# Performance work log

Hardware: AMD Instinct MI355X
Metric: run time of the kernel (lower is better)

The kernel has to match this reference:

```python
import math
import jax, jax.numpy as jnp
import numpy as np


def kaiser_sinc_filter1d(cutoff, half_width, kernel_size):
    even = kernel_size % 2 == 0
    half_size = kernel_size // 2
    delta_f = 4 * half_width
    A = 2.285 * (half_size - 1) * math.pi * delta_f + 7.95
    if A > 50.0:
        beta = 0.1102 * (A - 8.7)
    elif A >= 21.0:
        beta = 0.5842 * (A - 21) ** 0.4 + 0.07886 * (A - 21.0)
    else:
        beta = 0.0
    window = np.kaiser(kernel_size, beta)  # == torch.kaiser_window(periodic=False)
    if even:
        time = np.arange(-half_size, half_size) + 0.5
    else:
        time = np.arange(kernel_size) - half_size
    if cutoff == 0:
        filt = np.zeros_like(time)
    else:
        filt = 2 * cutoff * window * np.sinc(2 * cutoff * time)
        filt = filt / filt.sum()
    return jnp.asarray(filt, dtype=jnp.float32)  # [K]


def _depthwise_conv1d(x, filt, stride, lhs_dilation, padding):
    # x: [B, C, T]; filt: [K] shared across channels (groups=C depthwise)
    C = x.shape[1]
    K = filt.shape[0]
    w = jnp.broadcast_to(filt.reshape(1, 1, K), (C, 1, K))
    return jax.lax.conv_general_dilated(
        x, w,
        window_strides=(stride,),
        padding=[padding],
        lhs_dilation=(lhs_dilation,),
        dimension_numbers=("NCH", "OIH", "NCH"),
        feature_group_count=C,
    )


UP = 2
DOWN = 2
UP_K = 12
DOWN_K = 12


def setup_inputs() -> dict:
    key = jax.random.key(0)
    B, C, T = 16, 512, 4096
    x = jax.random.normal(key, (B, C, T), dtype=jnp.float32)
    alpha = jnp.zeros((1, C, 1), dtype=jnp.float32)
    beta = jnp.zeros((1, C, 1), dtype=jnp.float32)
    up_filter = kaiser_sinc_filter1d(0.5 / UP, 0.6 / UP, UP_K)
    down_filter = kaiser_sinc_filter1d(0.5 / DOWN, 0.6 / DOWN, DOWN_K)
    return {"x": x, "alpha": alpha, "beta": beta,
            "up_filter": up_filter, "down_filter": down_filter}


def reference(x, alpha, beta, up_filter, down_filter):
    # ---- UpSample1d(ratio=UP, kernel_size=UP_K) ----
    pad = UP_K // UP - 1
    pad_left = pad * UP + (UP_K - UP) // 2
    pad_right = pad * UP + (UP_K - UP + 1) // 2
    xp = jnp.pad(x, ((0, 0), (0, 0), (pad, pad)), mode="edge")  # replicate pad
    # conv_transpose1d(stride=UP) == conv with lhs_dilation=UP, full padding, flipped kernel
    y = UP * _depthwise_conv1d(xp, up_filter[::-1], stride=1,
                               lhs_dilation=UP, padding=(UP_K - 1, UP_K - 1))
    y = y[..., pad_left:-pad_right]  # [B, C, UP*T]

    # ---- SnakeBeta ----
    y = y + 1.0 / (jnp.exp(beta) + 1e-9) * jnp.square(jnp.sin(y * jnp.exp(alpha)))

    # ---- DownSample1d(ratio=DOWN, kernel_size=DOWN_K) via LowPassFilter1d ----
    even = DOWN_K % 2 == 0
    dpl = DOWN_K // 2 - int(even)
    dpr = DOWN_K // 2
    yp = jnp.pad(y, ((0, 0), (0, 0), (dpl, dpr)), mode="edge")
    out = _depthwise_conv1d(yp, down_filter, stride=DOWN,
                            lhs_dilation=1, padding=(0, 0))  # [B, C, T]
    return out
```

## Files before the change

### kernel.cpp

```cpp
#include <hip/hip_runtime.h>
#include <math.h>


#define T_LEN 4096
#define TILE  1024
#define NT    256
#define BPR   (T_LEN / TILE)
#define XT4   260
#define NG    258
#define PL4   260

__global__ __launch_bounds__(NT) void aa_act_kernel(
    const float* __restrict__ x,
    const float* __restrict__ alpha,
    const float* __restrict__ beta,
    const float* __restrict__ upf,
    const float* __restrict__ downf,
    float* __restrict__ out,
    int C)
{
    __shared__ __align__(16) float sx[XT4 * 4];
    __shared__ __align__(16) float sE[PL4 * 4];
    __shared__ __align__(16) float sO[PL4 * 4];

    const int tid = threadIdx.x;
    const int blk = blockIdx.x;
    const int row = blk >> 2;
    const int o0  = (blk & (BPR - 1)) * TILE;
    const int c   = row % C;

    const float* __restrict__ xr = x + (size_t)row * T_LEN;
    float* __restrict__ outr = out + (size_t)row * T_LEN;

    float u[12], d[12];
#pragma unroll
    for (int i = 0; i < 12; ++i) { u[i] = upf[i]; d[i] = downf[i]; }

    const float ea = __expf(alpha[c]);
    const float rb = 1.0f / (__expf(beta[c]) + 1e-9f);

    const bool eblk = (o0 == 0) || (o0 + TILE == T_LEN);
    for (int i4 = tid; i4 < XT4; i4 += NT) {
        int gi = o0 - 8 + 4 * i4;
        float4 v;
        if (!eblk || (unsigned)gi <= (unsigned)(T_LEN - 4)) {
            v = *(const float4*)(xr + gi);
        } else {
            v.x = xr[min(max(gi + 0, 0), T_LEN - 1)];
            v.y = xr[min(max(gi + 1, 0), T_LEN - 1)];
            v.z = xr[min(max(gi + 2, 0), T_LEN - 1)];
            v.w = xr[min(max(gi + 3, 0), T_LEN - 1)];
        }
        ((float4*)sx)[i4] = v;
    }
    __syncthreads();

    const float4* sx4 = (const float4*)sx;
    for (int g = tid; g < NG; g += NT) {
        float4 A = sx4[g], Bv = sx4[g + 1], Cv = sx4[g + 2];
        float f[12] = { A.x, A.y, A.z, A.w, Bv.x, Bv.y, Bv.z, Bv.w,
                        Cv.x, Cv.y, Cv.z, Cv.w };
        float eo[4], oo[4];
#pragma unroll
        for (int r = 0; r < 4; ++r) {
            float yo = f[r + 3] * u[10];
            yo = fmaf(f[r + 4], u[8], yo);
            yo = fmaf(f[r + 5], u[6], yo);
            yo = fmaf(f[r + 6], u[4], yo);
            yo = fmaf(f[r + 7], u[2], yo);
            yo = fmaf(f[r + 8], u[0], yo);
            float ye = f[r + 3] * u[11];
            ye = fmaf(f[r + 4], u[9], ye);
            ye = fmaf(f[r + 5], u[7], ye);
            ye = fmaf(f[r + 6], u[5], ye);
            ye = fmaf(f[r + 7], u[3], ye);
            ye = fmaf(f[r + 8], u[1], ye);
            yo *= 2.0f; ye *= 2.0f;
            float so_ = __sinf(yo * ea);
            float se_ = __sinf(ye * ea);
            oo[r] = fmaf(rb * so_, so_, yo);
            eo[r] = fmaf(rb * se_, se_, ye);
        }
        float4 ev; ev.x = eo[0]; ev.y = eo[1]; ev.z = eo[2]; ev.w = eo[3];
        float4 ov; ov.x = oo[0]; ov.y = oo[1]; ov.z = oo[2]; ov.w = oo[3];
        ((float4*)sE)[g] = ev;
        ((float4*)sO)[g] = ov;
    }
    __syncthreads();

    if (o0 == 0) {
        float L = sE[2];
        if (tid < 2) sE[tid] = L;
        if (tid < 3) sO[tid] = L;
    }
    if (o0 + TILE == T_LEN) {
        float R = sO[TILE + 2];
        if (tid < 6) sE[TILE + 2 + tid] = R;
        if (tid < 5) sO[TILE + 3 + tid] = R;
    }
    __syncthreads();

    const float4* e4 = (const float4*)sE;
    const float4* q4 = (const float4*)sO;
    float4 E0 = e4[tid], E1 = e4[tid + 1], E2 = e4[tid + 2];
    float4 O0 = q4[tid], O1 = q4[tid + 1], O2 = q4[tid + 2];
    float e[12] = { E0.x, E0.y, E0.z, E0.w, E1.x, E1.y, E1.z, E1.w,
                    E2.x, E2.y, E2.z, E2.w };
    float o_[12] = { O0.x, O0.y, O0.z, O0.w, O1.x, O1.y, O1.z, O1.w,
                     O2.x, O2.y, O2.z, O2.w };
    float acc[4];
#pragma unroll
    for (int r = 0; r < 4; ++r) {
        float a = e[r] * d[1];
        a = fmaf(e[r + 1], d[3],  a);
        a = fmaf(e[r + 2], d[5],  a);
        a = fmaf(e[r + 3], d[7],  a);
        a = fmaf(e[r + 4], d[9],  a);
        a = fmaf(e[r + 5], d[11], a);
        a = fmaf(o_[r],     d[0],  a);
        a = fmaf(o_[r + 1], d[2],  a);
        a = fmaf(o_[r + 2], d[4],  a);
        a = fmaf(o_[r + 3], d[6],  a);
        a = fmaf(o_[r + 4], d[8],  a);
        a = fmaf(o_[r + 5], d[10], a);
        acc[r] = a;
    }
    float4 o4; o4.x = acc[0]; o4.y = acc[1]; o4.z = acc[2]; o4.w = acc[3];
    ((float4*)(outr + o0))[tid] = o4;
}

extern "C" void kernel_launch(void* const* d_in, const int* in_sizes, int n_in,
                              void* d_out, int out_size, void* d_ws, size_t ws_size,
                              hipStream_t stream) {
    const float* x     = (const float*)d_in[0];
    const float* alpha = (const float*)d_in[1];
    const float* beta  = (const float*)d_in[2];
    const float* upf   = (const float*)d_in[3];
    const float* downf = (const float*)d_in[4];
    float* out = (float*)d_out;

    const int C    = in_sizes[1];
    const int rows = in_sizes[0] / T_LEN;

    dim3 grid(rows * BPR), block(NT);
    hipLaunchKernelGGL(aa_act_kernel, grid, block, 0, stream,
                       x, alpha, beta, upf, downf, out, C);
}
```

Measured before the change: 243.6 us.

## Compute each 16-output window per thread in registers, dropping shared memory

Result: slower. 270.4 us (+11.0%).

```diff
diff --git a/kernel.cpp b/kernel.cpp
--- a/kernel.cpp
+++ b/kernel.cpp
@@ -3,12 +3,8 @@
 
 
 #define T_LEN 4096
-#define TILE  1024
 #define NT    256
-#define BPR   (T_LEN / TILE)
-#define XT4   260
-#define NG    258
-#define PL4   260
+#define W     16
 
 __global__ __launch_bounds__(NT) void aa_act_kernel(
     const float* __restrict__ x,
@@ -19,98 +15,72 @@
     float* __restrict__ out,
     int C)
 {
-    __shared__ __align__(16) float sx[XT4 * 4];
-    __shared__ __align__(16) float sE[PL4 * 4];
-    __shared__ __align__(16) float sO[PL4 * 4];
-
-    const int tid = threadIdx.x;
-    const int blk = blockIdx.x;
-    const int row = blk >> 2;
-    const int o0  = (blk & (BPR - 1)) * TILE;
+    const int t   = threadIdx.x;
+    const int row = blockIdx.x;
     const int c   = row % C;
+    const int o0  = t * W;
 
     const float* __restrict__ xr = x + (size_t)row * T_LEN;
-    float* __restrict__ outr = out + (size_t)row * T_LEN;
+    float* __restrict__ outr     = out + (size_t)row * T_LEN;
 
-    float u[12], d[12];
+    float ue[6], uo[6], d[12];
 #pragma unroll
-    for (int i = 0; i < 12; ++i) { u[i] = upf[i]; d[i] = downf[i]; }
+    for (int m = 0; m < 6; ++m) {
+        ue[m] = 2.0f * upf[11 - 2 * m];
+        uo[m] = 2.0f * upf[10 - 2 * m];
+    }
+#pragma unroll
+    for (int i = 0; i < 12; ++i) d[i] = downf[i];
 
     const float ea = __expf(alpha[c]);
     const float rb = 1.0f / (__expf(beta[c]) + 1e-9f);
 
-    const bool eblk = (o0 == 0) || (o0 + TILE == T_LEN);
-    for (int i4 = tid; i4 < XT4; i4 += NT) {
-        int gi = o0 - 8 + 4 * i4;
-        float4 v;
-        if (!eblk || (unsigned)gi <= (unsigned)(T_LEN - 4)) {
-            v = *(const float4*)(xr + gi);
-        } else {
-            v.x = xr[min(max(gi + 0, 0), T_LEN - 1)];
-            v.y = xr[min(max(gi + 1, 0), T_LEN - 1)];
-            v.z = xr[min(max(gi + 2, 0), T_LEN - 1)];
-            v.w = xr[min(max(gi + 3, 0), T_LEN - 1)];
-        }
-        ((float4*)sx)[i4] = v;
+    float f[32];
+    if (t != 0 && t != NT - 1) {
+        const float4* p = (const float4*)(xr + o0 - 8);
+#pragma unroll
+        for (int i = 0; i < 8; ++i) ((float4*)f)[i] = p[i];
+    } else {
+#pragma unroll
+        for (int i = 0; i < 32; ++i)
+            f[i] = xr[min(max(o0 - 8 + i, 0), T_LEN - 1)];
     }
-    __syncthreads();
 
-    const float4* sx4 = (const float4*)sx;
-    for (int g = tid; g < NG; g += NT) {
-        float4 A = sx4[g], Bv = sx4[g + 1], Cv = sx4[g + 2];
-        float f[12] = { A.x, A.y, A.z, A.w, Bv.x, Bv.y, Bv.z, Bv.w,
-                        Cv.x, Cv.y, Cv.z, Cv.w };
-        float eo[4], oo[4];
+    float e[21], o_[21];
 #pragma unroll
-        for (int r = 0; r < 4; ++r) {
-            float yo = f[r + 3] * u[10];
-            yo = fmaf(f[r + 4], u[8], yo);
-            yo = fmaf(f[r + 5], u[6], yo);
-            yo = fmaf(f[r + 6], u[4], yo);
-            yo = fmaf(f[r + 7], u[2], yo);
-            yo = fmaf(f[r + 8], u[0], yo);
-            float ye = f[r + 3] * u[11];
-            ye = fmaf(f[r + 4], u[9], ye);
-            ye = fmaf(f[r + 5], u[7], ye);
-            ye = fmaf(f[r + 6], u[5], ye);
-            ye = fmaf(f[r + 7], u[3], ye);
-            ye = fmaf(f[r + 8], u[1], ye);
-            yo *= 2.0f; ye *= 2.0f;
-            float so_ = __sinf(yo * ea);
-            float se_ = __sinf(ye * ea);
-            oo[r] = fmaf(rb * so_, so_, yo);
-            eo[r] = fmaf(rb * se_, se_, ye);
-        }
-        float4 ev; ev.x = eo[0]; ev.y = eo[1]; ev.z = eo[2]; ev.w = eo[3];
-        float4 ov; ov.x = oo[0]; ov.y = oo[1]; ov.z = oo[2]; ov.w = oo[3];
-        ((float4*)sE)[g] = ev;
-        ((float4*)sO)[g] = ov;
+    for (int i = 0; i < 21; ++i) {
+        float ye = f[i + 3] * ue[0];
+        ye = fmaf(f[i + 4], ue[1], ye);
+        ye = fmaf(f[i + 5], ue[2], ye);
+        ye = fmaf(f[i + 6], ue[3], ye);
+        ye = fmaf(f[i + 7], ue[4], ye);
+        ye = fmaf(f[i + 8], ue[5], ye);
+        float yo = f[i + 3] * uo[0];
+        yo = fmaf(f[i + 4], uo[1], yo);
+        yo = fmaf(f[i + 5], uo[2], yo);
+        yo = fmaf(f[i + 6], uo[3], yo);
+        yo = fmaf(f[i + 7], uo[4], yo);
+        yo = fmaf(f[i + 8], uo[5], yo);
+        float se = __sinf(ye * ea);
+        float so = __sinf(yo * ea);
+        e[i]  = fmaf(rb * se, se, ye);
+        o_[i] = fmaf(rb * so, so, yo);
     }
-    __syncthreads();
 
-    if (o0 == 0) {
-        float L = sE[2];
-        if (tid < 2) sE[tid] = L;
-        if (tid < 3) sO[tid] = L;
+    if (t == 0) {
+        float L = e[2];
+        e[0] = L; e[1] = L;
+        o_[0] = L; o_[1] = L; o_[2] = L;
     }
-    if (o0 + TILE == T_LEN) {
-        float R = sO[TILE + 2];
-        if (tid < 6) sE[TILE + 2 + tid] = R;
-        if (tid < 5) sO[TILE + 3 + tid] = R;
+    if (t == NT - 1) {
+        float R = o_[18];
+        e[18] = R; e[19] = R; e[20] = R;
+        o_[19] = R; o_[20] = R;
     }
-    __syncthreads();
 
-    const float4* e4 = (const float4*)sE;
-    const float4* q4 = (const float4*)sO;
-    float4 E0 = e4[tid], E1 = e4[tid + 1], E2 = e4[tid + 2];
-    float4 O0 = q4[tid], O1 = q4[tid + 1], O2 = q4[tid + 2];
-    float e[12] = { E0.x, E0.y, E0.z, E0.w, E1.x, E1.y, E1.z, E1.w,
-                    E2.x, E2.y, E2.z, E2.w };
-    float o_[12] = { O0.x, O0.y, O0.z, O0.w, O1.x, O1.y, O1.z, O1.w,
-                     O2.x, O2.y, O2.z, O2.w };
-    float acc[4];
+    float acc[W];
 #pragma unroll
-    for (int r = 0; r < 4; ++r) {
+    for (int r = 0; r < W; ++r) {
         float a = e[r] * d[1];
         a = fmaf(e[r + 1], d[3],  a);
         a = fmaf(e[r + 2], d[5],  a);
@@ -125,8 +95,10 @@
         a = fmaf(o_[r + 5], d[10], a);
         acc[r] = a;
     }
-    float4 o4; o4.x = acc[0]; o4.y = acc[1]; o4.z = acc[2]; o4.w = acc[3];
-    ((float4*)(outr + o0))[tid] = o4;
+
+#pragma unroll
+    for (int i = 0; i < 4; ++i)
+        ((float4*)(outr + o0))[i] = *(float4*)(acc + 4 * i);
 }
 
 extern "C" void kernel_launch(void* const* d_in, const int* in_sizes, int n_in,
@@ -142,7 +114,7 @@
     const int C    = in_sizes[1];
     const int rows = in_sizes[0] / T_LEN;
 
-    dim3 grid(rows * BPR), block(NT);
+    dim3 grid(rows), block(NT);
     hipLaunchKernelGGL(aa_act_kernel, grid, block, 0, stream,
                        x, alpha, beta, upf, downf, out, C);
 }
```
